# Kernel optimization log

Measured on AMD Instinct MI355X. Metric: run time of the kernel, lower is better.

The kernel has to match this reference:

```python
import jax, jax.numpy as jnp
import numpy as np

N_NODES = 50000
N_EDGES = 1600000
D_IN = 128
D_OUT = 128


def setup_inputs() -> dict:
    key = jax.random.key(0)
    ks = jax.random.split(key, 8)
    feat = jax.random.normal(ks[0], (N_NODES, D_IN), dtype=jnp.float32)
    src = jax.random.randint(ks[1], (N_EDGES,), 0, N_NODES, dtype=jnp.int32)
    dst = jax.random.randint(ks[2], (N_EDGES,), 0, N_NODES, dtype=jnp.int32)
    # Xavier-uniform-ish init for the two linear layers
    lim = float(np.sqrt(6.0 / (D_IN + D_OUT))) * float(np.sqrt(2.0))  # gain=relu
    W_self = jax.random.uniform(ks[3], (D_OUT, D_IN), jnp.float32, -lim, lim)
    b_self = jnp.zeros((D_OUT,), jnp.float32)
    W_neigh = jax.random.uniform(ks[4], (D_OUT, D_IN), jnp.float32, -lim, lim)
    b_neigh = jnp.zeros((D_OUT,), jnp.float32)
    return {
        "feat": feat, "src": src, "dst": dst,
        "W_self": W_self, "b_self": b_self,
        "W_neigh": W_neigh, "b_neigh": b_neigh,
    }


def reference(feat, src, dst, W_self, b_self, W_neigh, b_neigh):
    """GraphSAGE 'mean' aggregator, eval mode (feat_drop=0).

    in_feats == out_feats -> lin_before_mp is False:
      h_neigh = fc_neigh(mean_{u in N(v)} feat[u])
      rst     = fc_self(feat[v]) + h_neigh
    Zero in-degree nodes get a zero neighbor vector (DGL mean semantics).
    """
    n = feat.shape[0]
    msg = feat[src]                                            # [E, D_in] gather
    agg = jax.ops.segment_sum(msg, dst, num_segments=n)        # [N, D_in] scatter-add
    deg = jax.ops.segment_sum(jnp.ones_like(src, feat.dtype), dst, num_segments=n)
    h_neigh = agg / jnp.maximum(deg, 1.0)[:, None]             # segment mean
    h_neigh = h_neigh @ W_neigh.T + b_neigh                    # fc_neigh
    h_self = feat @ W_self.T + b_self                          # fc_self
    return h_self + h_neigh
```

## Files before the change

kernel.cpp:

```cpp
#include <hip/hip_runtime.h>
#include <hip/hip_fp16.h>

#define D 128
#define BLOCK 256
#define CAP 128
#define BINSH 7
#define MAXBINS 392
#define BCAP 6144
#define CHUNK 2048

typedef __attribute__((ext_vector_type(2))) float floatx2;
typedef __attribute__((ext_vector_type(4))) float floatx4;
typedef __attribute__((ext_vector_type(8))) _Float16 half8;

union U4H8 { uint4 u; half8 h; };

__global__ __launch_bounds__(256) void sage_cvt(
    const float4* __restrict__ feat4, unsigned int* __restrict__ feat8, int n4)
{
    int i = blockIdx.x * blockDim.x + threadIdx.x;
    if (i >= n4) return;
    float4 f = feat4[i];
    unsigned int r = __builtin_amdgcn_cvt_pk_fp8_f32(f.x, f.y, 0u, false);
    r = __builtin_amdgcn_cvt_pk_fp8_f32(f.z, f.w, r, true);
    feat8[i] = r;
}

__global__ __launch_bounds__(256) void sage_prepw(
    const float* __restrict__ W_self, const float* __restrict__ W_neigh,
    const float* __restrict__ b_self, const float* __restrict__ b_neigh,
    unsigned int* __restrict__ wcat2, float* __restrict__ biascat)
{
    int idx = blockIdx.x * blockDim.x + threadIdx.x;
    if (idx >= 128 * 128) return;
    int n = idx >> 7;
    int k = (idx & 127) * 2;
    float a, b;
    if (k < 128) { a = W_self[n * 128 + k];        b = W_self[n * 128 + k + 1]; }
    else         { a = W_neigh[n * 128 + k - 128]; b = W_neigh[n * 128 + k - 127]; }
    __half2 h = __floats2half2_rn(a, b);
    wcat2[idx] = *reinterpret_cast<unsigned int*>(&h);
    if (idx < 128) biascat[idx] = b_self[idx] + b_neigh[idx];
}

__global__ __launch_bounds__(256) void sage_bin(
    const int* __restrict__ src, const int* __restrict__ dst,
    int* __restrict__ bin_cursor, unsigned int* __restrict__ bins, int n_edges)
{
    __shared__ int hist[MAXBINS];
    __shared__ int base[MAXBINS];
    int t = threadIdx.x;
    if (t < MAXBINS - 256) hist[256 + t] = 0;
    hist[t] = 0;
    __syncthreads();

    int e0 = blockIdx.x * CHUNK;
    unsigned int item[8];
    int binr[8];
    #pragma unroll
    for (int k = 0; k < 8; ++k) {
        int i = e0 + k * 256 + t;
        if (i < n_edges) {
            int d = dst[i];
            int s = src[i];
            int bin = d >> BINSH;
            int r = atomicAdd(&hist[bin], 1);
            item[k] = ((unsigned int)(d & 127) << 16) | (unsigned int)s;
            binr[k] = (bin << 16) | r;
        } else binr[k] = -1;
    }
    __syncthreads();
    #pragma unroll
    for (int bb = 0; bb < 2; ++bb) {
        int bin = t + bb * 256;
        if (bin < MAXBINS) {
            int h = hist[bin];
            base[bin] = h ? atomicAdd(&bin_cursor[bin], h) : 0;
        }
    }
    __syncthreads();
    #pragma unroll
    for (int k = 0; k < 8; ++k) {
        if (binr[k] >= 0) {
            int bin = binr[k] >> 16;
            int pos = base[bin] + (binr[k] & 0xFFFF);
            if (pos < BCAP)
                bins[(size_t)bin * BCAP + pos] = item[k];
        }
    }
}

__global__ __launch_bounds__(256) void sage_bucket(
    const unsigned int* __restrict__ bins, const int* __restrict__ bin_cursor,
    unsigned short* __restrict__ bucket, int* __restrict__ cnt_g, int n_nodes)
{
    __shared__ int cnt[128];
    __shared__ unsigned short buck[128 * CAP];
    int b = blockIdx.x;
    int t = threadIdx.x;
    if (t < 128) cnt[t] = 0;
    __syncthreads();

    int n_items = min(bin_cursor[b], BCAP);
    const unsigned int* bp = bins + (size_t)b * BCAP;
    for (int i = t; i < n_items; i += 256) {
        unsigned int it = bp[i];
        int d = it >> 16;
        int c = atomicAdd(&cnt[d], 1);
        if (c < CAP) buck[d * CAP + c] = (unsigned short)(it & 0xFFFFu);
    }
    __syncthreads();

    const uint4* lb = (const uint4*)buck;
    uint4* gb = (uint4*)(bucket + (size_t)b * 128 * CAP);
    #pragma unroll
    for (int k = 0; k < 8; ++k)
        gb[k * 256 + t] = lb[k * 256 + t];
    if (t < 128) {
        int node = b * 128 + t;
        if (node < n_nodes) cnt_g[node] = cnt[t];
    }
}

__device__ inline void addq(float* acc, unsigned int q) {
    floatx2 lo = __builtin_amdgcn_cvt_pk_f32_fp8(q, false);
    floatx2 hi = __builtin_amdgcn_cvt_pk_f32_fp8(q, true);
    acc[0] += lo[0]; acc[1] += lo[1]; acc[2] += hi[0]; acc[3] += hi[1];
}

__device__ inline void add16(float* acc, uint4 r) {
    addq(acc + 0,  r.x);
    addq(acc + 4,  r.y);
    addq(acc + 8,  r.z);
    addq(acc + 12, r.w);
}

__global__ __launch_bounds__(BLOCK) void sage_agg(
    const uint4* __restrict__ feat84,
    const int* __restrict__ cnt_g,
    const unsigned short* __restrict__ bucket,
    uint4* __restrict__ meanh4,
    int n_nodes)
{
    int v0 = blockIdx.x * 16;
    int t = threadIdx.x;
    int wave = t >> 6;
    int lane = t & 63;
    int g = (lane >> 4) & 3;
    int eo = (lane >> 3) & 1;
    int h = lane & 7;
    int lo = 2 * g + eo;

    for (int v = wave; v < 16; v += 4) {
        int node = v0 + v;
        if (node >= n_nodes) break;
        int deg = cnt_g[node];
        int cv = min(deg, CAP);
        const unsigned short* b = bucket + (size_t)node * CAP;

        float acc[16];
        #pragma unroll
        for (int i = 0; i < 16; ++i) acc[i] = 0.0f;

        int e = 0;
        for (; e + 32 <= cv; e += 32) {
            int s0 = b[e + lo];
            int s1 = b[e + 8 + lo];
            int s2 = b[e + 16 + lo];
            int s3 = b[e + 24 + lo];
            uint4 r0 = feat84[(size_t)s0 * 8 + h];
            uint4 r1 = feat84[(size_t)s1 * 8 + h];
            uint4 r2 = feat84[(size_t)s2 * 8 + h];
            uint4 r3 = feat84[(size_t)s3 * 8 + h];
            add16(acc, r0); add16(acc, r1); add16(acc, r2); add16(acc, r3);
        }
        #pragma unroll
        for (int k = 0; k < 4; ++k) {
            int idx = e + 8 * k + lo;
            if (idx < cv) {
                uint4 r = feat84[(size_t)b[idx] * 8 + h];
                add16(acc, r);
            }
        }

        #pragma unroll
        for (int i = 0; i < 16; ++i) {
            acc[i] += __shfl_xor(acc[i], 8);
            acc[i] += __shfl_xor(acc[i], 16);
            acc[i] += __shfl_xor(acc[i], 32);
        }
        if (lane < 8) {
            float inv = 1.0f / fmaxf((float)deg, 1.0f);
            unsigned int p[8];
            #pragma unroll
            for (int i = 0; i < 8; ++i) {
                __half2 hh = __floats2half2_rn(acc[2 * i] * inv, acc[2 * i + 1] * inv);
                p[i] = *reinterpret_cast<unsigned int*>(&hh);
            }
            uint4 lo4 = { p[0], p[1], p[2], p[3] };
            uint4 hi4 = { p[4], p[5], p[6], p[7] };
            meanh4[(size_t)node * 16 + h * 2]     = lo4;
            meanh4[(size_t)node * 16 + h * 2 + 1] = hi4;
        }
    }
}

__global__ __launch_bounds__(256) void sage_gemm(
    const float* __restrict__ feat,
    const uint4* __restrict__ meanh4,
    const uint4* __restrict__ wcat4,
    const float* __restrict__ biascat,
    float* __restrict__ out, int n_nodes)
{
    int t = threadIdx.x;
    int wave = t >> 6;
    int lane = t & 63;
    int m16 = lane & 15;
    int kq = lane >> 4;
    int rowbase = blockIdx.x * 64 + wave * 16;
    int m = rowbase + m16;
    int msafe = (m < n_nodes) ? m : 0;

    half8 a[8];
    const float4* fp = (const float4*)(feat + (size_t)msafe * D);
    #pragma unroll
    for (int kt = 0; kt < 4; ++kt) {
        float4 f0 = fp[kt * 8 + kq * 2];
        float4 f1 = fp[kt * 8 + kq * 2 + 1];
        half8 hh;
        hh[0] = (_Float16)f0.x; hh[1] = (_Float16)f0.y;
        hh[2] = (_Float16)f0.z; hh[3] = (_Float16)f0.w;
        hh[4] = (_Float16)f1.x; hh[5] = (_Float16)f1.y;
        hh[6] = (_Float16)f1.z; hh[7] = (_Float16)f1.w;
        a[kt] = hh;
    }
    const uint4* mp = meanh4 + (size_t)msafe * 16;
    #pragma unroll
    for (int kt = 0; kt < 4; ++kt) {
        U4H8 u; u.u = mp[kt * 4 + kq];
        a[4 + kt] = u.h;
    }

    #pragma unroll
    for (int ct = 0; ct < 8; ++ct) {
        floatx4 acc = { 0.f, 0.f, 0.f, 0.f };
        #pragma unroll
        for (int kt = 0; kt < 8; ++kt) {
            U4H8 w; w.u = wcat4[(size_t)(ct * 16 + m16) * 32 + kt * 4 + kq];
            acc = __builtin_amdgcn_mfma_f32_16x16x32_f16(a[kt], w.h, acc, 0, 0, 0);
        }
        float bias = biascat[ct * 16 + m16];
        #pragma unroll
        for (int i = 0; i < 4; ++i) {
            int r = rowbase + kq * 4 + i;
            if (r < n_nodes)
                out[(size_t)r * D + ct * 16 + m16] = acc[i] + bias;
        }
    }
}

extern "C" void kernel_launch(void* const* d_in, const int* in_sizes, int n_in,
                              void* d_out, int out_size, void* d_ws, size_t ws_size,
                              hipStream_t stream)
{
    const float* feat    = (const float*)d_in[0];
    const int*   src     = (const int*)d_in[1];
    const int*   dst     = (const int*)d_in[2];
    const float* W_self  = (const float*)d_in[3];
    const float* b_self  = (const float*)d_in[4];
    const float* W_neigh = (const float*)d_in[5];
    const float* b_neigh = (const float*)d_in[6];
    float* out = (float*)d_out;

    int n_nodes = in_sizes[0] / D;
    int n_edges = in_sizes[1];
    int nbins = (n_nodes + 127) >> 7;

    unsigned short* bucket = (unsigned short*)d_ws;
    int* cnt_g = (int*)(bucket + (size_t)nbins * 128 * CAP);
    unsigned int* feat8 = (unsigned int*)(cnt_g + n_nodes);
    unsigned int* meanh = feat8 + (size_t)n_nodes * (D / 4);
    unsigned int* wcat = meanh + (size_t)n_nodes * (D / 2);
    float* biascat = (float*)(wcat + 128 * 128);
    int* bin_cursor = (int*)(biascat + 128);

    unsigned int* bins = (unsigned int*)d_out;

    hipMemsetAsync(bin_cursor, 0, MAXBINS * sizeof(int), stream);

    {
        int n4 = n_nodes * (D / 4);
        sage_cvt<<<(n4 + 255) / 256, 256, 0, stream>>>(
            (const float4*)feat, feat8, n4);
    }
    sage_prepw<<<(128 * 128 + 255) / 256, 256, 0, stream>>>(
        W_self, W_neigh, b_self, b_neigh, wcat, biascat);
    sage_bin<<<(n_edges + CHUNK - 1) / CHUNK, 256, 0, stream>>>(
        src, dst, bin_cursor, bins, n_edges);
    sage_bucket<<<nbins, 256, 0, stream>>>(
        bins, bin_cursor, bucket, cnt_g, n_nodes);
    sage_agg<<<(n_nodes + 15) / 16, BLOCK, 0, stream>>>(
        (const uint4*)feat8, cnt_g, bucket, (uint4*)meanh, n_nodes);
    sage_gemm<<<(n_nodes + 63) / 64, 256, 0, stream>>>(
        feat, (const uint4*)meanh, (const uint4*)wcat, biascat, out, n_nodes);
}
```

Before: 217.6 us.

## Fuse aggregation with GEMM via LDS and merge prep kernels

The mean-aggregation kernel now keeps each block's 16 mean rows in shared memory and runs the fp16 MFMA projection in the same kernel, with each wave computing two output column tiles. This drops the global meanh buffer round trip and one launch. Separately, the fp8 feature conversion, weight packing and bin-cursor zeroing are merged into one prep kernel, replacing a memset and two launches. In exchange, each GEMM block now covers 16 rows instead of 64, so the feature rows are still read from global memory and weights are reloaded by four times as many blocks.

```diff
diff --git a/kernel.cpp b/kernel.cpp
--- a/kernel.cpp
+++ b/kernel.cpp
@@ -15,32 +15,36 @@
 
 union U4H8 { uint4 u; half8 h; };
 
-__global__ __launch_bounds__(256) void sage_cvt(
-    const float4* __restrict__ feat4, unsigned int* __restrict__ feat8, int n4)
-{
-    int i = blockIdx.x * blockDim.x + threadIdx.x;
-    if (i >= n4) return;
-    float4 f = feat4[i];
-    unsigned int r = __builtin_amdgcn_cvt_pk_fp8_f32(f.x, f.y, 0u, false);
-    r = __builtin_amdgcn_cvt_pk_fp8_f32(f.z, f.w, r, true);
-    feat8[i] = r;
-}
-
-__global__ __launch_bounds__(256) void sage_prepw(
+__global__ __launch_bounds__(256) void sage_prep(
+    const float4* __restrict__ feat4, unsigned int* __restrict__ feat8, int n4,
+    int ncvt_blocks,
     const float* __restrict__ W_self, const float* __restrict__ W_neigh,
     const float* __restrict__ b_self, const float* __restrict__ b_neigh,
-    unsigned int* __restrict__ wcat2, float* __restrict__ biascat)
-{
-    int idx = blockIdx.x * blockDim.x + threadIdx.x;
-    if (idx >= 128 * 128) return;
-    int n = idx >> 7;
-    int k = (idx & 127) * 2;
-    float a, b;
-    if (k < 128) { a = W_self[n * 128 + k];        b = W_self[n * 128 + k + 1]; }
-    else         { a = W_neigh[n * 128 + k - 128]; b = W_neigh[n * 128 + k - 127]; }
-    __half2 h = __floats2half2_rn(a, b);
-    wcat2[idx] = *reinterpret_cast<unsigned int*>(&h);
-    if (idx < 128) biascat[idx] = b_self[idx] + b_neigh[idx];
+    unsigned int* __restrict__ wcat2, float* __restrict__ biascat,
+    int* __restrict__ bin_cursor)
+{
+    int b = blockIdx.x, t = threadIdx.x;
+    if (b < ncvt_blocks) {
+        int i = b * 256 + t;
+        if (i < n4) {
+            float4 f = feat4[i];
+            unsigned int r = __builtin_amdgcn_cvt_pk_fp8_f32(f.x, f.y, 0u, false);
+            r = __builtin_amdgcn_cvt_pk_fp8_f32(f.z, f.w, r, true);
+            feat8[i] = r;
+        }
+    } else if (b < ncvt_blocks + 64) {
+        int idx = (b - ncvt_blocks) * 256 + t;
+        int n = idx >> 7;
+        int k = (idx & 127) * 2;
+        float a, bb;
+        if (k < 128) { a = W_self[n * 128 + k];        bb = W_self[n * 128 + k + 1]; }
+        else         { a = W_neigh[n * 128 + k - 128]; bb = W_neigh[n * 128 + k - 127]; }
+        __half2 h = __floats2half2_rn(a, bb);
+        wcat2[idx] = *reinterpret_cast<unsigned int*>(&h);
+        if (idx < 128) biascat[idx] = b_self[idx] + b_neigh[idx];
+    } else {
+        for (int i = t; i < MAXBINS; i += 256) bin_cursor[i] = 0;
+    }
 }
 
 __global__ __launch_bounds__(256) void sage_bin(
@@ -135,126 +139,126 @@
     addq(acc + 12, r.w);
 }
 
-__global__ __launch_bounds__(BLOCK) void sage_agg(
+__global__ __launch_bounds__(BLOCK) void sage_agg_gemm(
+    const float* __restrict__ feat,
     const uint4* __restrict__ feat84,
     const int* __restrict__ cnt_g,
     const unsigned short* __restrict__ bucket,
-    uint4* __restrict__ meanh4,
-    int n_nodes)
-{
+    const uint4* __restrict__ wcat4,
+    const float* __restrict__ biascat,
+    float* __restrict__ out, int n_nodes)
+{
+    __shared__ _Float16 mean_lds[16][136];
+
     int v0 = blockIdx.x * 16;
     int t = threadIdx.x;
     int wave = t >> 6;
     int lane = t & 63;
-    int g = (lane >> 4) & 3;
-    int eo = (lane >> 3) & 1;
-    int h = lane & 7;
-    int lo = 2 * g + eo;
-
-    for (int v = wave; v < 16; v += 4) {
-        int node = v0 + v;
-        if (node >= n_nodes) break;
-        int deg = cnt_g[node];
-        int cv = min(deg, CAP);
-        const unsigned short* b = bucket + (size_t)node * CAP;
-
-        float acc[16];
+
+    {
+        int g = (lane >> 4) & 3;
+        int eo = (lane >> 3) & 1;
+        int h = lane & 7;
+        int lo = 2 * g + eo;
+
+        for (int v = wave; v < 16; v += 4) {
+            int node = v0 + v;
+            if (node >= n_nodes) break;
+            int deg = cnt_g[node];
+            int cv = min(deg, CAP);
+            const unsigned short* b = bucket + (size_t)node * CAP;
+
+            float acc[16];
+            #pragma unroll
+            for (int i = 0; i < 16; ++i) acc[i] = 0.0f;
+
+            int e = 0;
+            for (; e + 32 <= cv; e += 32) {
+                int s0 = b[e + lo];
+                int s1 = b[e + 8 + lo];
+                int s2 = b[e + 16 + lo];
+                int s3 = b[e + 24 + lo];
+                uint4 r0 = feat84[(size_t)s0 * 8 + h];
+                uint4 r1 = feat84[(size_t)s1 * 8 + h];
+                uint4 r2 = feat84[(size_t)s2 * 8 + h];
+                uint4 r3 = feat84[(size_t)s3 * 8 + h];
+                add16(acc, r0); add16(acc, r1); add16(acc, r2); add16(acc, r3);
+            }
+            #pragma unroll
+            for (int k = 0; k < 4; ++k) {
+                int idx = e + 8 * k + lo;
+                if (idx < cv) {
+                    uint4 r = feat84[(size_t)b[idx] * 8 + h];
+                    add16(acc, r);
+                }
+            }
+
+            #pragma unroll
+            for (int i = 0; i < 16; ++i) {
+                acc[i] += __shfl_xor(acc[i], 8);
+                acc[i] += __shfl_xor(acc[i], 16);
+                acc[i] += __shfl_xor(acc[i], 32);
+            }
+            if (lane < 8) {
+                float inv = 1.0f / fmaxf((float)deg, 1.0f);
+                unsigned int p[8];
+                #pragma unroll
+                for (int i = 0; i < 8; ++i) {
+                    __half2 hh = __floats2half2_rn(acc[2 * i] * inv, acc[2 * i + 1] * inv);
+                    p[i] = *reinterpret_cast<unsigned int*>(&hh);
+                }
+                uint4 lo4 = { p[0], p[1], p[2], p[3] };
+                uint4 hi4 = { p[4], p[5], p[6], p[7] };
+                uint4* xp = (uint4*)&mean_lds[v][h * 16];
+                xp[0] = lo4;
+                xp[1] = hi4;
+            }
+        }
+    }
+    __syncthreads();
+
+    {
+        int m16 = lane & 15;
+        int kq = lane >> 4;
+        int m = v0 + m16;
+        int msafe = (m < n_nodes) ? m : 0;
+
+        half8 a[8];
+        const float4* fp = (const float4*)(feat + (size_t)msafe * D);
         #pragma unroll
-        for (int i = 0; i < 16; ++i) acc[i] = 0.0f;
-
-        int e = 0;
-        for (; e + 32 <= cv; e += 32) {
-            int s0 = b[e + lo];
-            int s1 = b[e + 8 + lo];
-            int s2 = b[e + 16 + lo];
-            int s3 = b[e + 24 + lo];
-            uint4 r0 = feat84[(size_t)s0 * 8 + h];
-            uint4 r1 = feat84[(size_t)s1 * 8 + h];
-            uint4 r2 = feat84[(size_t)s2 * 8 + h];
-            uint4 r3 = feat84[(size_t)s3 * 8 + h];
-            add16(acc, r0); add16(acc, r1); add16(acc, r2); add16(acc, r3);
-        }
+        for (int kt = 0; kt < 4; ++kt) {
+            float4 f0 = fp[kt * 8 + kq * 2];
+            float4 f1 = fp[kt * 8 + kq * 2 + 1];
+            half8 hh;
+            hh[0] = (_Float16)f0.x; hh[1] = (_Float16)f0.y;
+            hh[2] = (_Float16)f0.z; hh[3] = (_Float16)f0.w;
+            hh[4] = (_Float16)f1.x; hh[5] = (_Float16)f1.y;
+            hh[6] = (_Float16)f1.z; hh[7] = (_Float16)f1.w;
+            a[kt] = hh;
+        }
+        const uint4* mrow = (const uint4*)&mean_lds[m16][0];
         #pragma unroll
-        for (int k = 0; k < 4; ++k) {
-            int idx = e + 8 * k + lo;
-            if (idx < cv) {
-                uint4 r = feat84[(size_t)b[idx] * 8 + h];
-                add16(acc, r);
-            }
+        for (int kt = 0; kt < 4; ++kt) {
+            U4H8 u; u.u = mrow[kt * 4 + kq];
+            a[4 + kt] = u.h;
         }
 
         #pragma unroll
-        for (int i = 0; i < 16; ++i) {
-            acc[i] += __shfl_xor(acc[i], 8);
-            acc[i] += __shfl_xor(acc[i], 16);
-            acc[i] += __shfl_xor(acc[i], 32);
-        }
-        if (lane < 8) {
-            float inv = 1.0f / fmaxf((float)deg, 1.0f);
-            unsigned int p[8];
-            #pragma unroll
-            for (int i = 0; i < 8; ++i) {
-                __half2 hh = __floats2half2_rn(acc[2 * i] * inv, acc[2 * i + 1] * inv);
-                p[i] = *reinterpret_cast<unsigned int*>(&hh);
-            }
-            uint4 lo4 = { p[0], p[1], p[2], p[3] };
-            uint4 hi4 = { p[4], p[5], p[6], p[7] };
-            meanh4[(size_t)node * 16 + h * 2]     = lo4;
-            meanh4[(size_t)node * 16 + h * 2 + 1] = hi4;
-        }
-    }
-}
-
-__global__ __launch_bounds__(256) void sage_gemm(
-    const float* __restrict__ feat,
-    const uint4* __restrict__ meanh4,
-    const uint4* __restrict__ wcat4,
-    const float* __restrict__ biascat,
-    float* __restrict__ out, int n_nodes)
-{
-    int t = threadIdx.x;
-    int wave = t >> 6;
-    int lane = t & 63;
-    int m16 = lane & 15;
-    int kq = lane >> 4;
-    int rowbase = blockIdx.x * 64 + wave * 16;
-    int m = rowbase + m16;
-    int msafe = (m < n_nodes) ? m : 0;
-
-    half8 a[8];
-    const float4* fp = (const float4*)(feat + (size_t)msafe * D);
-    #pragma unroll
-    for (int kt = 0; kt < 4; ++kt) {
-        float4 f0 = fp[kt * 8 + kq * 2];
-        float4 f1 = fp[kt * 8 + kq * 2 + 1];
-        half8 hh;
-        hh[0] = (_Float16)f0.x; hh[1] = (_Float16)f0.y;
-        hh[2] = (_Float16)f0.z; hh[3] = (_Float16)f0.w;
-        hh[4] = (_Float16)f1.x; hh[5] = (_Float16)f1.y;
-        hh[6] = (_Float16)f1.z; hh[7] = (_Float16)f1.w;
-        a[kt] = hh;
-    }
-    const uint4* mp = meanh4 + (size_t)msafe * 16;
-    #pragma unroll
-    for (int kt = 0; kt < 4; ++kt) {
-        U4H8 u; u.u = mp[kt * 4 + kq];
-        a[4 + kt] = u.h;
-    }
-
-    #pragma unroll
-    for (int ct = 0; ct < 8; ++ct) {
-        floatx4 acc = { 0.f, 0.f, 0.f, 0.f };
-        #pragma unroll
-        for (int kt = 0; kt < 8; ++kt) {
-            U4H8 w; w.u = wcat4[(size_t)(ct * 16 + m16) * 32 + kt * 4 + kq];
-            acc = __builtin_amdgcn_mfma_f32_16x16x32_f16(a[kt], w.h, acc, 0, 0, 0);
-        }
-        float bias = biascat[ct * 16 + m16];
-        #pragma unroll
-        for (int i = 0; i < 4; ++i) {
-            int r = rowbase + kq * 4 + i;
-            if (r < n_nodes)
-                out[(size_t)r * D + ct * 16 + m16] = acc[i] + bias;
+        for (int cc = 0; cc < 2; ++cc) {
+            int ct = wave * 2 + cc;
+            floatx4 acc = { 0.f, 0.f, 0.f, 0.f };
+            #pragma unroll
+            for (int kt = 0; kt < 8; ++kt) {
+                U4H8 w; w.u = wcat4[(size_t)(ct * 16 + m16) * 32 + kt * 4 + kq];
+                acc = __builtin_amdgcn_mfma_f32_16x16x32_f16(a[kt], w.h, acc, 0, 0, 0);
+            }
+            float bias = biascat[ct * 16 + m16];
+            #pragma unroll
+            for (int i = 0; i < 4; ++i) {
+                int r = v0 + kq * 4 + i;
+                if (r < n_nodes)
+                    out[(size_t)r * D + ct * 16 + m16] = acc[i] + bias;
+            }
         }
     }
 }
@@ -279,28 +283,22 @@
     unsigned short* bucket = (unsigned short*)d_ws;
     int* cnt_g = (int*)(bucket + (size_t)nbins * 128 * CAP);
     unsigned int* feat8 = (unsigned int*)(cnt_g + n_nodes);
-    unsigned int* meanh = feat8 + (size_t)n_nodes * (D / 4);
-    unsigned int* wcat = meanh + (size_t)n_nodes * (D / 2);
+    unsigned int* wcat = feat8 + (size_t)n_nodes * (D / 4);
     float* biascat = (float*)(wcat + 128 * 128);
     int* bin_cursor = (int*)(biascat + 128);
 
     unsigned int* bins = (unsigned int*)d_out;
 
-    hipMemsetAsync(bin_cursor, 0, MAXBINS * sizeof(int), stream);
-
-    {
-        int n4 = n_nodes * (D / 4);
-        sage_cvt<<<(n4 + 255) / 256, 256, 0, stream>>>(
-            (const float4*)feat, feat8, n4);
-    }
-    sage_prepw<<<(128 * 128 + 255) / 256, 256, 0, stream>>>(
-        W_self, W_neigh, b_self, b_neigh, wcat, biascat);
+    int n4 = n_nodes * (D / 4);
+    int ncvt = (n4 + 255) / 256;
+    sage_prep<<<ncvt + 64 + 1, 256, 0, stream>>>(
+        (const float4*)feat, feat8, n4, ncvt,
+        W_self, W_neigh, b_self, b_neigh, wcat, biascat, bin_cursor);
     sage_bin<<<(n_edges + CHUNK - 1) / CHUNK, 256, 0, stream>>>(
         src, dst, bin_cursor, bins, n_edges);
     sage_bucket<<<nbins, 256, 0, stream>>>(
         bins, bin_cursor, bucket, cnt_g, n_nodes);
-    sage_agg<<<(n_nodes + 15) / 16, BLOCK, 0, stream>>>(
-        (const uint4*)feat8, cnt_g, bucket, (uint4*)meanh, n_nodes);
-    sage_gemm<<<(n_nodes + 63) / 64, 256, 0, stream>>>(
-        feat, (const uint4*)meanh, (const uint4*)wcat, biascat, out, n_nodes);
-}
+    sage_agg_gemm<<<(n_nodes + 15) / 16, BLOCK, 0, stream>>>(
+        feat, (const uint4*)feat8, cnt_g, bucket,
+        (const uint4*)wcat, biascat, out, n_nodes);
+}
```

Result: faster. 209.2 us (-3.9%).
